# Optimization experiments

Hardware: AMD Instinct MI355X
Metric: run time of the kernel (lower is better)

The kernel has to match this reference:

```python
import jax, jax.numpy as jnp
import numpy as np

B, S, D, H = 2, 2048, 1024, 16
DK = D // H  # 64


def setup_inputs() -> dict:
    key = jax.random.key(0)
    ks = jax.random.split(key, 8)
    sc = 1.0 / np.sqrt(D)
    return {
        "q": jax.random.normal(ks[0], (B, S, D), jnp.float32),
        "k": jax.random.normal(ks[1], (B, S, D), jnp.float32),
        "v": jax.random.normal(ks[2], (B, S, D), jnp.float32),
        "Wq": jax.random.normal(ks[3], (D, D), jnp.float32) * sc,
        "bq": jnp.zeros((D,), jnp.float32),
        "Wk": jax.random.normal(ks[4], (D, D), jnp.float32) * sc,
        "bk": jnp.zeros((D,), jnp.float32),
        "Wv": jax.random.normal(ks[5], (D, D), jnp.float32) * sc,
        "bv": jnp.zeros((D,), jnp.float32),
        "Wo": jax.random.normal(ks[6], (D, D), jnp.float32) * sc,
        "bo": jnp.zeros((D,), jnp.float32),
    }


def _heads(x, W, b):
    # torch nn.Linear: x @ W.T + b, then view(bs,-1,H,DK).transpose(1,2)
    bsz, seq, _ = x.shape
    y = x @ W.T + b
    return y.reshape(bsz, seq, H, DK).transpose(0, 2, 1, 3)  # [B,H,S,DK]


def reference(q, k, v, Wq, bq, Wk, bk, Wv, bv, Wo, bo):
    qh = _heads(q, Wq, bq)
    kh = _heads(k, Wk, bk)
    vh = _heads(v, Wv, bv)
    # scores: [B,H,S,S]; intended scale 1/sqrt(d_k) (source passes tensor k as d_k by mistake)
    scores = jnp.einsum("bhqd,bhkd->bhqk", qh, kh) / jnp.sqrt(jnp.float32(DK))
    attn = jax.nn.softmax(scores, axis=-1)  # dropout is identity in eval
    ctx = jnp.einsum("bhqk,bhkd->bhqd", attn, vh)  # [B,H,S,DK]
    concat = ctx.transpose(0, 2, 1, 3).reshape(-1, H * DK)  # [B*S, D] (source flattens batch+seq)
    return concat @ Wo.T + bo
```

## Files before the change

### kernel.cpp

```cpp
#include <hip/hip_runtime.h>

typedef __attribute__((ext_vector_type(4))) float f32x4;
typedef __attribute__((ext_vector_type(8))) short short8;
typedef __attribute__((ext_vector_type(4))) unsigned short u16x4;
typedef __attribute__((ext_vector_type(2))) unsigned u32x2;
typedef __attribute__((ext_vector_type(4))) unsigned u32x4;

#define DEV static __device__ __forceinline__

#define BSZ 2
#define SEQ 2048
#define DMODEL 1024
#define NH 16
#define DKH 64
#define MROWS (BSZ*SEQ)
#define HEAD_ELEMS (BSZ*NH*SEQ*DKH)
#define WMAT_ELEMS (DMODEL*DMODEL)
#define QSCALE 0.18033688011111374f

DEV unsigned short f2bf(float f) {
    unsigned u = __builtin_bit_cast(unsigned, f);
    u += 0x7FFFu + ((u >> 16) & 1u);
    return (unsigned short)(u >> 16);
}

DEV unsigned cvtpk(float a, float b) {
    unsigned r;
    asm("v_cvt_pk_bf16_f32 %0, %1, %2" : "=v"(r) : "v"(a), "v"(b));
    return r;
}

DEV float fexp2(float x) {
#if __has_builtin(__builtin_amdgcn_exp2f)
    return __builtin_amdgcn_exp2f(x);
#else
    float r;
    asm("v_exp_f32 %0, %1\n\ts_nop 0" : "=v"(r) : "v"(x));
    return r;
#endif
}

DEV void gload16(const void* g, void* l) {
    __builtin_amdgcn_global_load_lds(
        (const __attribute__((address_space(1))) void*)g,
        (__attribute__((address_space(3))) void*)l, 16, 0, 0);
}

__global__ __launch_bounds__(256) void convall_kernel(
    const float* __restrict__ q, const float* __restrict__ k,
    const float* __restrict__ v,
    const float* __restrict__ Wq, const float* __restrict__ Wk,
    const float* __restrict__ Wv, const float* __restrict__ Wo,
    unsigned short* __restrict__ abf, unsigned short* __restrict__ wbf)
{
    const int z = blockIdx.y;
    const int i = (blockIdx.x * 256 + threadIdx.x) * 8;
    const float* src;
    unsigned short* dst;
    if (z < 3) {
        src = ((z == 0) ? q : (z == 1) ? k : v) + i;
        dst = abf + (size_t)z * HEAD_ELEMS + i;
    } else {
        const int mi = i >> 20;
        const int off = i & (WMAT_ELEMS - 1);
        src = ((mi == 0) ? Wq : (mi == 1) ? Wk : (mi == 2) ? Wv : Wo) + off;
        dst = wbf + i;
    }
    f32x4 a = *(const f32x4*)(src);
    f32x4 b = *(const f32x4*)(src + 4);
    u32x4 o;
    o[0] = cvtpk(a[0], a[1]); o[1] = cvtpk(a[2], a[3]);
    o[2] = cvtpk(b[0], b[1]); o[3] = cvtpk(b[2], b[3]);
    *(u32x4*)(dst) = o;
}

__global__ __launch_bounds__(256) void wconv_kernel(
    const float* __restrict__ Wq, const float* __restrict__ Wk,
    const float* __restrict__ Wv, const float* __restrict__ Wo,
    unsigned short* __restrict__ dst)
{
    const int z = blockIdx.y;
    const float* src = (z == 0) ? Wq : (z == 1) ? Wk : (z == 2) ? Wv : Wo;
    const int i = (blockIdx.x * 256 + threadIdx.x) * 4;
    f32x4 v = *(const f32x4*)(src + i);
    u16x4 o;
    o[0] = f2bf(v[0]); o[1] = f2bf(v[1]); o[2] = f2bf(v[2]); o[3] = f2bf(v[3]);
    *(u16x4*)(dst + (size_t)z * WMAT_ELEMS + i) = o;
}

__global__ __launch_bounds__(256) void aconv_kernel(
    const float* __restrict__ src, unsigned short* __restrict__ dst)
{
    const int i = (blockIdx.x * 256 + threadIdx.x) * 8;
    f32x4 a = *(const f32x4*)(src + i);
    f32x4 b = *(const f32x4*)(src + i + 4);
    u32x4 o;
    o[0] = cvtpk(a[0], a[1]); o[1] = cvtpk(a[2], a[3]);
    o[2] = cvtpk(b[0], b[1]); o[3] = cvtpk(b[2], b[3]);
    *(u32x4*)(dst + i) = o;
}

__global__ __launch_bounds__(256, 3) void proj_gemm_kernel(
    const unsigned short* __restrict__ Aq, const unsigned short* __restrict__ Ak,
    const unsigned short* __restrict__ Av,
    const unsigned short* __restrict__ Wbf,
    const float* __restrict__ bq, const float* __restrict__ bk, const float* __restrict__ bvv,
    unsigned short* __restrict__ heads, int zbase)
{
    const int z = zbase + blockIdx.z;
    const unsigned short* A = (z == 0) ? Aq : (z == 1) ? Ak : Av;
    const float* bias = (z == 0) ? bq : (z == 1) ? bk : bvv;
    const unsigned short* W = Wbf + (size_t)z * WMAT_ELEMS;
    unsigned short* outp = heads + (size_t)z * HEAD_ELEMS;

    __shared__ __align__(16) unsigned short As[128 * 64];
    __shared__ __align__(16) unsigned short Bs[128 * 64];

    const int tid = threadIdx.x;
    const int lane = tid & 63;
    const int w = tid >> 6;
    const int wr = w >> 1, wc = w & 1;
    const int l15 = lane & 15, l4 = lane >> 4;
    const int m0 = blockIdx.x * 128, n0 = blockIdx.y * 128;

    f32x4 acc[4][4];
    #pragma unroll
    for (int i = 0; i < 4; i++)
        #pragma unroll
        for (int j = 0; j < 4; j++) acc[i][j] = (f32x4){0.f, 0.f, 0.f, 0.f};

    const int srow = w * 8 + (lane >> 3);
    const int ssrc = ((lane & 7) ^ (srow & 7)) * 8;
    const unsigned short* ga = A + (size_t)(m0 + srow) * DMODEL + ssrc;
    const unsigned short* gb = W + (size_t)(n0 + srow) * DMODEL + ssrc;

    for (int k0 = 0; k0 < DMODEL; k0 += 64) {
        __syncthreads();
        #pragma unroll
        for (int c = 0; c < 4; c++) {
            gload16(ga + (size_t)c * 32 * DMODEL + k0, As + (c * 4 + w) * 512);
            gload16(gb + (size_t)c * 32 * DMODEL + k0, Bs + (c * 4 + w) * 512);
        }
        __syncthreads();

        short8 af[2][4], bf[2][4];
        #pragma unroll
        for (int mi = 0; mi < 4; mi++) {
            const int r = wr * 64 + mi * 16 + l15;
            const int x = r & 7;
            const char* base = (const char*)As + r * 128;
            af[0][mi] = *(const short8*)(base + ((l4 ^ x) << 4));
            af[1][mi] = *(const short8*)(base + (((4 + l4) ^ x) << 4));
        }
        #pragma unroll
        for (int ni = 0; ni < 4; ni++) {
            const int r = wc * 64 + ni * 16 + l15;
            const int x = r & 7;
            const char* base = (const char*)Bs + r * 128;
            bf[0][ni] = *(const short8*)(base + ((l4 ^ x) << 4));
            bf[1][ni] = *(const short8*)(base + (((4 + l4) ^ x) << 4));
        }

        __builtin_amdgcn_s_setprio(1);
        #pragma unroll
        for (int ks = 0; ks < 2; ks++)
            #pragma unroll
            for (int mi = 0; mi < 4; mi++)
                #pragma unroll
                for (int ni = 0; ni < 4; ni++)
                    acc[mi][ni] = __builtin_amdgcn_mfma_f32_16x16x32_bf16(
                        af[ks][mi], bf[ks][ni], acc[mi][ni], 0, 0, 0);
        __builtin_amdgcn_s_setprio(0);
    }

    if (z < 2) {
        const float sc = (z == 0) ? QSCALE : 1.0f;
        #pragma unroll
        for (int ni = 0; ni < 4; ni++) {
            const int n = n0 + wc * 64 + ni * 16 + l15;
            const float bn = bias[n];
            const int h = n >> 6, dk = n & 63;
            #pragma unroll
            for (int mi = 0; mi < 4; mi++) {
                #pragma unroll
                for (int r = 0; r < 4; r++) {
                    const int m = m0 + wr * 64 + mi * 16 + l4 * 4 + r;
                    const int b = m >> 11, s = m & 2047;
                    outp[((size_t)((b * NH + h) * SEQ) + s) * DKH + dk] =
                        f2bf((acc[mi][ni][r] + bn) * sc);
                }
            }
        }
    } else {
        #pragma unroll
        for (int ni = 0; ni < 4; ni++) {
            const int n = n0 + wc * 64 + ni * 16 + l15;
            const float bn = bias[n];
            const int h = n >> 6, dk = n & 63;
            #pragma unroll
            for (int mi = 0; mi < 4; mi++) {
                const int m = m0 + wr * 64 + mi * 16 + l4 * 4;
                const int b = m >> 11, s = m & 2047;
                float v0 = acc[mi][ni][0] + bn, v1 = acc[mi][ni][1] + bn;
                float v2 = acc[mi][ni][2] + bn, v3 = acc[mi][ni][3] + bn;
                u32x2 pk; pk[0] = cvtpk(v0, v1); pk[1] = cvtpk(v2, v3);
                *(u32x2*)(outp + ((size_t)((b * NH + h) * DKH + dk)) * SEQ + s) = pk;
            }
        }
    }
}

#define KVB 64
#define NTILES (SEQ/KVB)

__global__ __launch_bounds__(256, 4) void attn_kernel(
    const unsigned short* __restrict__ Qh, const unsigned short* __restrict__ Kh,
    const unsigned short* __restrict__ Vtg, unsigned short* __restrict__ Ctx)
{
    __shared__ __align__(16) char lds[40960];

    const int tid = threadIdx.x;
    const int lane = tid & 63, w = tid >> 6;
    const int l15 = lane & 15, l4 = lane >> 4;

    const int bid = blockIdx.x;
    const int bh = (bid & 7) * 4 + (bid >> 8);
    const int qt = (bid >> 3) & 31;
    const int q0 = qt * 64;

    const unsigned short* Qp = Qh + (size_t)bh * (SEQ * DKH);
    const unsigned short* Kp = Kh + (size_t)bh * (SEQ * DKH);
    const unsigned short* Vp = Vtg + (size_t)bh * (SEQ * DKH);
    char* Pw = lds + 32768 + w * 2048;

    const unsigned short* qrow = Qp + (size_t)(q0 + w * 16 + l15) * DKH + l4 * 8;
    const short8 qf0 = *(const short8*)(qrow);
    const short8 qf1 = *(const short8*)(qrow + 32);

    const int srow = tid >> 3;
    const int sseg = ((tid & 7) ^ (srow & 7)) * 8;
    const unsigned short* kg = Kp + (size_t)srow * DKH + sseg;
    const unsigned short* vg = Vp + (size_t)srow * SEQ + sseg;

    float lsum = 0.f;
    f32x4 o[4];
    #pragma unroll
    for (int d = 0; d < 4; d++) o[d] = (f32x4){0.f, 0.f, 0.f, 0.f};

    const int fb = l15 * 128 + ((l4 * 16) ^ ((l15 & 7) << 4));
    const int pswz = (l15 & 7) << 4;

    #pragma unroll
    for (int r = 0; r < 2; r++) {
        gload16(kg + (size_t)r * 32 * DKH,         lds + r * 4096 + w * 1024);
        gload16(vg + (size_t)r * 32 * SEQ, lds + 16384 + r * 4096 + w * 1024);
    }

    for (int t = 0; t < NTILES; ++t) {
        __syncthreads();
        const int cur = t & 1;

        if (t + 1 < NTILES) {
            const unsigned short* kn = kg + (size_t)(t + 1) * (KVB * DKH);
            const unsigned short* vn = vg + (t + 1) * KVB;
            char* kd = lds + (cur ^ 1) * 8192 + w * 1024;
            char* vd = lds + 16384 + (cur ^ 1) * 8192 + w * 1024;
            #pragma unroll
            for (int r = 0; r < 2; r++) {
                gload16(kn + (size_t)r * 32 * DKH, kd + r * 4096);
                gload16(vn + (size_t)r * 32 * SEQ, vd + r * 4096);
            }
        }

        const char* Kb = lds + cur * 8192;
        const char* Vb = lds + 16384 + cur * 8192;

        f32x4 s[4];
        #pragma unroll
        for (int nf = 0; nf < 4; nf++) s[nf] = (f32x4){0.f, 0.f, 0.f, 0.f};
        __builtin_amdgcn_s_setprio(1);
        #pragma unroll
        for (int ks = 0; ks < 2; ks++) {
            const int fo = fb ^ (ks << 6);
            #pragma unroll
            for (int nf = 0; nf < 4; nf++) {
                short8 kf = *(const short8*)(Kb + fo + nf * 2048);
                s[nf] = __builtin_amdgcn_mfma_f32_16x16x32_bf16(
                    kf, ks ? qf1 : qf0, s[nf], 0, 0, 0);
            }
        }
        __builtin_amdgcn_s_setprio(0);

        float ps = 0.f;
        #pragma unroll
        for (int nf = 0; nf < 4; nf++) {
            const float p0 = fexp2(s[nf][0]), p1 = fexp2(s[nf][1]);
            const float p2 = fexp2(s[nf][2]), p3 = fexp2(s[nf][3]);
            ps += (p0 + p1) + (p2 + p3);
            u32x2 pk;
            pk[0] = cvtpk(p0, p1);
            pk[1] = cvtpk(p2, p3);
            *(u32x2*)(Pw + l15 * 128 + ((nf * 32 + l4 * 8) ^ pswz)) = pk;
        }
        ps += __shfl_xor(ps, 16);
        ps += __shfl_xor(ps, 32);
        lsum += ps;

        __builtin_amdgcn_s_setprio(1);
        #pragma unroll
        for (int ks = 0; ks < 2; ks++) {
            short8 pa = *(const short8*)(Pw + l15 * 128 + ((ks * 64 + l4 * 16) ^ pswz));
            const int fo = fb ^ (ks << 6);
            #pragma unroll
            for (int d = 0; d < 4; d++) {
                short8 vb = *(const short8*)(Vb + fo + d * 2048);
                o[d] = __builtin_amdgcn_mfma_f32_16x16x32_bf16(pa, vb, o[d], 0, 0, 0);
            }
        }
        __builtin_amdgcn_s_setprio(0);
    }

    const int b = bh >> 4, h = bh & 15;
    const float linv = 1.f / lsum;
    #pragma unroll
    for (int r = 0; r < 4; r++) {
        const float lr = __shfl(linv, l4 * 4 + r);
        const int sq = q0 + w * 16 + l4 * 4 + r;
        const size_t base = ((size_t)(b * SEQ + sq)) * DMODEL + h * DKH;
        #pragma unroll
        for (int d = 0; d < 4; d++)
            Ctx[base + d * 16 + l15] = f2bf(o[d][r] * lr);
    }
}

__global__ __launch_bounds__(256, 3) void out_gemm_kernel(
    const unsigned short* __restrict__ Ctx, const unsigned short* __restrict__ Wobf,
    const float* __restrict__ bo, float* __restrict__ outp)
{
    __shared__ __align__(16) unsigned short As[128 * 64];
    __shared__ __align__(16) unsigned short Bs[128 * 64];

    const int tid = threadIdx.x;
    const int lane = tid & 63;
    const int w = tid >> 6;
    const int wr = w >> 1, wc = w & 1;
    const int l15 = lane & 15, l4 = lane >> 4;
    const int m0 = blockIdx.x * 128, n0 = blockIdx.y * 128;

    f32x4 acc[4][4];
    #pragma unroll
    for (int i = 0; i < 4; i++)
        #pragma unroll
        for (int j = 0; j < 4; j++) acc[i][j] = (f32x4){0.f, 0.f, 0.f, 0.f};

    const int srow = w * 8 + (lane >> 3);
    const int ssrc = ((lane & 7) ^ (srow & 7)) * 8;
    const unsigned short* ga = Ctx + (size_t)(m0 + srow) * DMODEL + ssrc;
    const unsigned short* gb = Wobf + (size_t)(n0 + srow) * DMODEL + ssrc;

    for (int k0 = 0; k0 < DMODEL; k0 += 64) {
        __syncthreads();
        #pragma unroll
        for (int c = 0; c < 4; c++) {
            gload16(ga + (size_t)c * 32 * DMODEL + k0, As + (c * 4 + w) * 512);
            gload16(gb + (size_t)c * 32 * DMODEL + k0, Bs + (c * 4 + w) * 512);
        }
        __syncthreads();

        short8 af[2][4], bf[2][4];
        #pragma unroll
        for (int mi = 0; mi < 4; mi++) {
            const int r = wr * 64 + mi * 16 + l15;
            const int x = r & 7;
            const char* base = (const char*)As + r * 128;
            af[0][mi] = *(const short8*)(base + ((l4 ^ x) << 4));
            af[1][mi] = *(const short8*)(base + (((4 + l4) ^ x) << 4));
        }
        #pragma unroll
        for (int ni = 0; ni < 4; ni++) {
            const int r = wc * 64 + ni * 16 + l15;
            const int x = r & 7;
            const char* base = (const char*)Bs + r * 128;
            bf[0][ni] = *(const short8*)(base + ((l4 ^ x) << 4));
            bf[1][ni] = *(const short8*)(base + (((4 + l4) ^ x) << 4));
        }

        __builtin_amdgcn_s_setprio(1);
        #pragma unroll
        for (int ks = 0; ks < 2; ks++)
            #pragma unroll
            for (int mi = 0; mi < 4; mi++)
                #pragma unroll
                for (int ni = 0; ni < 4; ni++)
                    acc[mi][ni] = __builtin_amdgcn_mfma_f32_16x16x32_bf16(
                        af[ks][mi], bf[ks][ni], acc[mi][ni], 0, 0, 0);
        __builtin_amdgcn_s_setprio(0);
    }

    #pragma unroll
    for (int ni = 0; ni < 4; ni++) {
        const int n = n0 + wc * 64 + ni * 16 + l15;
        const float bn = bo[n];
        #pragma unroll
        for (int mi = 0; mi < 4; mi++) {
            #pragma unroll
            for (int r = 0; r < 4; r++) {
                const int m = m0 + wr * 64 + mi * 16 + l4 * 4 + r;
                outp[(size_t)m * DMODEL + n] = acc[mi][ni][r] + bn;
            }
        }
    }
}

extern "C" void kernel_launch(void* const* d_in, const int* in_sizes, int n_in,
                              void* d_out, int out_size, void* d_ws, size_t ws_size,
                              hipStream_t stream)
{
    (void)in_sizes; (void)n_in; (void)out_size;
    const float* q  = (const float*)d_in[0];
    const float* k  = (const float*)d_in[1];
    const float* v  = (const float*)d_in[2];
    const float* Wq = (const float*)d_in[3];
    const float* bq = (const float*)d_in[4];
    const float* Wk = (const float*)d_in[5];
    const float* bk = (const float*)d_in[6];
    const float* Wv = (const float*)d_in[7];
    const float* bv = (const float*)d_in[8];
    const float* Wo = (const float*)d_in[9];
    const float* bo = (const float*)d_in[10];
    float* outp = (float*)d_out;

    unsigned short* ws  = (unsigned short*)d_ws;
    unsigned short* Wbf = ws;

    const size_t BIG_NEED = (size_t)(4u * WMAT_ELEMS + 6u * HEAD_ELEMS) * 2u;

    if (ws_size >= BIG_NEED) {
        unsigned short* qbf = ws + 4u * WMAT_ELEMS;
        unsigned short* kbf = qbf + HEAD_ELEMS;
        unsigned short* vbf = kbf + HEAD_ELEMS;
        unsigned short* Qh  = vbf + HEAD_ELEMS;
        unsigned short* Kh  = Qh + HEAD_ELEMS;
        unsigned short* Vt  = Kh + HEAD_ELEMS;
        unsigned short* Ctx = qbf;

        hipLaunchKernelGGL(convall_kernel, dim3(2048, 4), dim3(256), 0, stream,
                           q, k, v, Wq, Wk, Wv, Wo, qbf, Wbf);
        hipLaunchKernelGGL(proj_gemm_kernel, dim3(32, 8, 3), dim3(256), 0, stream,
                           qbf, kbf, vbf, Wbf, bq, bk, bv, Qh, 0);
        hipLaunchKernelGGL(attn_kernel, dim3(1024), dim3(256), 0, stream,
                           Qh, Kh, Vt, Ctx);
        hipLaunchKernelGGL(out_gemm_kernel, dim3(32, 8), dim3(256), 0, stream,
                           Ctx, Wbf + 3u * WMAT_ELEMS, bo, outp);
    } else {
        unsigned short* Abf = ws + 4u * WMAT_ELEMS;
        unsigned short* Qh  = Abf + HEAD_ELEMS;
        unsigned short* Kh  = Qh + HEAD_ELEMS;
        unsigned short* Vt  = Kh + HEAD_ELEMS;
        unsigned short* Ctx = Abf;

        hipLaunchKernelGGL(wconv_kernel, dim3(1024, 4), dim3(256), 0, stream,
                           Wq, Wk, Wv, Wo, Wbf);
        const float* srcs[3] = {q, k, v};
        for (int z = 0; z < 3; z++) {
            hipLaunchKernelGGL(aconv_kernel, dim3(2048), dim3(256), 0, stream, srcs[z], Abf);
            hipLaunchKernelGGL(proj_gemm_kernel, dim3(32, 8, 1), dim3(256), 0, stream,
                               Abf, Abf, Abf, Wbf, bq, bk, bv, Qh, z);
        }
        hipLaunchKernelGGL(attn_kernel, dim3(1024), dim3(256), 0, stream,
                           Qh, Kh, Vt, Ctx);
        hipLaunchKernelGGL(out_gemm_kernel, dim3(32, 8), dim3(256), 0, stream,
                           Ctx, Wbf + 3u * WMAT_ELEMS, bo, outp);
    }
}
```

Baseline: 117.1 us.

## Switch attention to 32x32x16 MFMA with register-resident P via permlane swaps

Rewrites the attention kernel to use 2 waves per block, each covering 32 query rows with 32x32x16 bf16 MFMAs instead of 16x16x32 tiles. The P matrix is no longer staged through LDS: it is repacked in registers with v_permlane32_swap so the exp'd scores feed straight into the PV MFMA as the A operand. This removes the P LDS round-trip and its buffer, and cuts one cross-lane reduction. In exchange, each block has fewer waves for latency hiding, each thread issues more K/V load instructions per tile, and accumulator register pressure goes up.

```diff
diff --git a/kernel.cpp b/kernel.cpp
--- a/kernel.cpp
+++ b/kernel.cpp
@@ -1,6 +1,7 @@
 #include <hip/hip_runtime.h>
 
 typedef __attribute__((ext_vector_type(4))) float f32x4;
+typedef __attribute__((ext_vector_type(16))) float f32x16;
 typedef __attribute__((ext_vector_type(8))) short short8;
 typedef __attribute__((ext_vector_type(4))) unsigned short u16x4;
 typedef __attribute__((ext_vector_type(2))) unsigned u32x2;
@@ -38,6 +39,11 @@
     asm("v_exp_f32 %0, %1\n\ts_nop 0" : "=v"(r) : "v"(x));
     return r;
 #endif
+}
+
+DEV void plswap(unsigned& a, unsigned& b) {
+    asm volatile("s_nop 1\n\tv_permlane32_swap_b32 %0, %1\n\ts_nop 1"
+                 : "+v"(a), "+v"(b));
 }
 
 DEV void gload16(const void* g, void* l) {
@@ -213,15 +219,15 @@
 #define KVB 64
 #define NTILES (SEQ/KVB)
 
-__global__ __launch_bounds__(256, 4) void attn_kernel(
+__global__ __launch_bounds__(128, 2) void attn_kernel(
     const unsigned short* __restrict__ Qh, const unsigned short* __restrict__ Kh,
     const unsigned short* __restrict__ Vtg, unsigned short* __restrict__ Ctx)
 {
-    __shared__ __align__(16) char lds[40960];
+    __shared__ __align__(16) char lds[32768];
 
     const int tid = threadIdx.x;
     const int lane = tid & 63, w = tid >> 6;
-    const int l15 = lane & 15, l4 = lane >> 4;
+    const int l31 = lane & 31, l1 = lane >> 5;
 
     const int bid = blockIdx.x;
     const int bh = (bid & 7) * 4 + (bid >> 8);
@@ -231,29 +237,29 @@
     const unsigned short* Qp = Qh + (size_t)bh * (SEQ * DKH);
     const unsigned short* Kp = Kh + (size_t)bh * (SEQ * DKH);
     const unsigned short* Vp = Vtg + (size_t)bh * (SEQ * DKH);
-    char* Pw = lds + 32768 + w * 2048;
-
-    const unsigned short* qrow = Qp + (size_t)(q0 + w * 16 + l15) * DKH + l4 * 8;
-    const short8 qf0 = *(const short8*)(qrow);
-    const short8 qf1 = *(const short8*)(qrow + 32);
-
-    const int srow = tid >> 3;
-    const int sseg = ((tid & 7) ^ (srow & 7)) * 8;
-    const unsigned short* kg = Kp + (size_t)srow * DKH + sseg;
-    const unsigned short* vg = Vp + (size_t)srow * SEQ + sseg;
+
+    const char* qrow = (const char*)(Qp + (size_t)(q0 + w * 32 + l31) * DKH);
+    short8 qf[4];
+    #pragma unroll
+    for (int m = 0; m < 4; m++)
+        qf[m] = *(const short8*)(qrow + m * 32 + l1 * 16);
+
+    const int srow8 = tid >> 3;
+    const int sseg = ((tid & 7) ^ (srow8 & 7)) * 8;
+    const unsigned short* kg = Kp + (size_t)srow8 * DKH + sseg;
+    const unsigned short* vg = Vp + (size_t)srow8 * SEQ + sseg;
+    char* kd0 = lds         + w * 1024;
+    char* vd0 = lds + 16384 + w * 1024;
 
     float lsum = 0.f;
-    f32x4 o[4];
-    #pragma unroll
-    for (int d = 0; d < 4; d++) o[d] = (f32x4){0.f, 0.f, 0.f, 0.f};
-
-    const int fb = l15 * 128 + ((l4 * 16) ^ ((l15 & 7) << 4));
-    const int pswz = (l15 & 7) << 4;
-
-    #pragma unroll
-    for (int r = 0; r < 2; r++) {
-        gload16(kg + (size_t)r * 32 * DKH,         lds + r * 4096 + w * 1024);
-        gload16(vg + (size_t)r * 32 * SEQ, lds + 16384 + r * 4096 + w * 1024);
+    f32x16 o0 = {}, o1 = {};
+
+    const int x7 = l31 & 7;
+
+    #pragma unroll
+    for (int r = 0; r < 4; r++) {
+        gload16(kg + (size_t)r * 16 * DKH, kd0 + r * 2048);
+        gload16(vg + (size_t)r * 16 * SEQ, vd0 + r * 2048);
     }
 
     for (int t = 0; t < NTILES; ++t) {
@@ -266,56 +272,60 @@
             char* kd = lds + (cur ^ 1) * 8192 + w * 1024;
             char* vd = lds + 16384 + (cur ^ 1) * 8192 + w * 1024;
             #pragma unroll
-            for (int r = 0; r < 2; r++) {
-                gload16(kn + (size_t)r * 32 * DKH, kd + r * 4096);
-                gload16(vn + (size_t)r * 32 * SEQ, vd + r * 4096);
+            for (int r = 0; r < 4; r++) {
+                gload16(kn + (size_t)r * 16 * DKH, kd + r * 2048);
+                gload16(vn + (size_t)r * 16 * SEQ, vd + r * 2048);
             }
         }
 
         const char* Kb = lds + cur * 8192;
         const char* Vb = lds + 16384 + cur * 8192;
 
-        f32x4 s[4];
-        #pragma unroll
-        for (int nf = 0; nf < 4; nf++) s[nf] = (f32x4){0.f, 0.f, 0.f, 0.f};
+        f32x16 s0 = {}, s1 = {};
         __builtin_amdgcn_s_setprio(1);
         #pragma unroll
-        for (int ks = 0; ks < 2; ks++) {
-            const int fo = fb ^ (ks << 6);
-            #pragma unroll
-            for (int nf = 0; nf < 4; nf++) {
-                short8 kf = *(const short8*)(Kb + fo + nf * 2048);
-                s[nf] = __builtin_amdgcn_mfma_f32_16x16x32_bf16(
-                    kf, ks ? qf1 : qf0, s[nf], 0, 0, 0);
-            }
+        for (int m = 0; m < 4; m++) {
+            const int co = ((m * 2 + l1) ^ x7) << 4;
+            short8 kf0 = *(const short8*)(Kb + l31 * 128 + co);
+            short8 kf1 = *(const short8*)(Kb + (32 + l31) * 128 + co);
+            s0 = __builtin_amdgcn_mfma_f32_32x32x16_bf16(kf0, qf[m], s0, 0, 0, 0);
+            s1 = __builtin_amdgcn_mfma_f32_32x32x16_bf16(kf1, qf[m], s1, 0, 0, 0);
         }
         __builtin_amdgcn_s_setprio(0);
 
         float ps = 0.f;
-        #pragma unroll
-        for (int nf = 0; nf < 4; nf++) {
-            const float p0 = fexp2(s[nf][0]), p1 = fexp2(s[nf][1]);
-            const float p2 = fexp2(s[nf][2]), p3 = fexp2(s[nf][3]);
-            ps += (p0 + p1) + (p2 + p3);
-            u32x2 pk;
-            pk[0] = cvtpk(p0, p1);
-            pk[1] = cvtpk(p2, p3);
-            *(u32x2*)(Pw + l15 * 128 + ((nf * 32 + l4 * 8) ^ pswz)) = pk;
-        }
-        ps += __shfl_xor(ps, 16);
+        short8 pf[4];
+        #pragma unroll
+        for (int kt = 0; kt < 2; kt++) {
+            float p[16];
+            #pragma unroll
+            for (int r = 0; r < 16; r++) {
+                p[r] = fexp2(kt ? s1[r] : s0[r]);
+                ps += p[r];
+            }
+            #pragma unroll
+            for (int sl = 0; sl < 2; sl++) {
+                unsigned a0 = cvtpk(p[8 * sl + 0], p[8 * sl + 1]);
+                unsigned a1 = cvtpk(p[8 * sl + 2], p[8 * sl + 3]);
+                unsigned b0 = cvtpk(p[8 * sl + 4], p[8 * sl + 5]);
+                unsigned b1 = cvtpk(p[8 * sl + 6], p[8 * sl + 7]);
+                plswap(a0, b0);
+                plswap(a1, b1);
+                u32x4 fr; fr[0] = a0; fr[1] = a1; fr[2] = b0; fr[3] = b1;
+                pf[kt * 2 + sl] = __builtin_bit_cast(short8, fr);
+            }
+        }
         ps += __shfl_xor(ps, 32);
         lsum += ps;
 
         __builtin_amdgcn_s_setprio(1);
         #pragma unroll
-        for (int ks = 0; ks < 2; ks++) {
-            short8 pa = *(const short8*)(Pw + l15 * 128 + ((ks * 64 + l4 * 16) ^ pswz));
-            const int fo = fb ^ (ks << 6);
-            #pragma unroll
-            for (int d = 0; d < 4; d++) {
-                short8 vb = *(const short8*)(Vb + fo + d * 2048);
-                o[d] = __builtin_amdgcn_mfma_f32_16x16x32_bf16(pa, vb, o[d], 0, 0, 0);
-            }
+        for (int s = 0; s < 4; s++) {
+            const int co = ((s * 2 + l1) ^ x7) << 4;
+            short8 vb0 = *(const short8*)(Vb + l31 * 128 + co);
+            short8 vb1 = *(const short8*)(Vb + (32 + l31) * 128 + co);
+            o0 = __builtin_amdgcn_mfma_f32_32x32x16_bf16(pf[s], vb0, o0, 0, 0, 0);
+            o1 = __builtin_amdgcn_mfma_f32_32x32x16_bf16(pf[s], vb1, o1, 0, 0, 0);
         }
         __builtin_amdgcn_s_setprio(0);
     }
@@ -323,13 +333,12 @@
     const int b = bh >> 4, h = bh & 15;
     const float linv = 1.f / lsum;
     #pragma unroll
-    for (int r = 0; r < 4; r++) {
-        const float lr = __shfl(linv, l4 * 4 + r);
-        const int sq = q0 + w * 16 + l4 * 4 + r;
-        const size_t base = ((size_t)(b * SEQ + sq)) * DMODEL + h * DKH;
-        #pragma unroll
-        for (int d = 0; d < 4; d++)
-            Ctx[base + d * 16 + l15] = f2bf(o[d][r] * lr);
+    for (int r = 0; r < 16; r++) {
+        const int qrw = (r & 3) + 8 * (r >> 2) + 4 * l1;
+        const float lr = __shfl(linv, qrw);
+        const size_t base = ((size_t)(b * SEQ + q0 + w * 32 + qrw)) * DMODEL + h * DKH;
+        Ctx[base + l31]      = f2bf(o0[r] * lr);
+        Ctx[base + 32 + l31] = f2bf(o1[r] * lr);
     }
 }
 
@@ -448,7 +457,7 @@
                            q, k, v, Wq, Wk, Wv, Wo, qbf, Wbf);
         hipLaunchKernelGGL(proj_gemm_kernel, dim3(32, 8, 3), dim3(256), 0, stream,
                            qbf, kbf, vbf, Wbf, bq, bk, bv, Qh, 0);
-        hipLaunchKernelGGL(attn_kernel, dim3(1024), dim3(256), 0, stream,
+        hipLaunchKernelGGL(attn_kernel, dim3(1024), dim3(128), 0, stream,
                            Qh, Kh, Vt, Ctx);
         hipLaunchKernelGGL(out_gemm_kernel, dim3(32, 8), dim3(256), 0, stream,
                            Ctx, Wbf + 3u * WMAT_ELEMS, bo, outp);
@@ -467,7 +476,7 @@
             hipLaunchKernelGGL(proj_gemm_kernel, dim3(32, 8, 1), dim3(256), 0, stream,
                                Abf, Abf, Abf, Wbf, bq, bk, bv, Qh, z);
         }
-        hipLaunchKernelGGL(attn_kernel, dim3(1024), dim3(256), 0, stream,
+        hipLaunchKernelGGL(attn_kernel, dim3(1024), dim3(128), 0, stream,
                            Qh, Kh, Vt, Ctx);
         hipLaunchKernelGGL(out_gemm_kernel, dim3(32, 8), dim3(256), 0, stream,
                            Ctx, Wbf + 3u * WMAT_ELEMS, bo, outp);
```

New measurement: 118.6 us. Within noise of the previous version (+1.2%).
